# Kernel optimization log

Measured on AMD Instinct MI355X. Metric: run time of the kernel, lower is better.

Reference implementation:

```python
import jax, jax.numpy as jnp
import numpy as np

EPS = 1e-5

def gather_neighbour(pc, idx):
    # pc: [B,N,d], idx: [B,Q,k] -> [B,Q,k,d]
    return jax.vmap(lambda p, i: p[i])(pc, idx)

def rel_pos_encoding(q_xyz, src_xyz, idx):
    # q_xyz: [B,Q,3], src_xyz: [B,N,3], idx: [B,Q,k] -> [B,Q,k,10]
    nbr = gather_neighbour(src_xyz, idx)              # [B,Q,k,3]
    tile = q_xyz[:, :, None, :]                       # [B,Q,1,3]
    rel = tile - nbr                                  # [B,Q,k,3]
    dis = jnp.sqrt(jnp.sum(rel * rel, axis=-1, keepdims=True))
    tile_b = jnp.broadcast_to(tile, nbr.shape)
    return jnp.concatenate([dis, rel, tile_b, nbr], axis=-1)

def conv_bn_relu(x, W, g, b, m, v):
    # 1x1 conv (bias-free) + inference BatchNorm + ReLU; x: [B,Q,K,Cin], W: [Cout,Cin]
    y = jnp.einsum('bqkc,oc->bqko', x, W)
    y = (y - m) * (g * jax.lax.rsqrt(v + EPS)) + b
    return jax.nn.relu(y)

def att_pool(x, Wfc, Wm, g, b, m, v):
    # x: [B,Q,K,C] -> [B,Q,1,Cout]; softmax over neighbor axis K
    att = jnp.einsum('bqkc,oc->bqko', x, Wfc)
    att = jax.nn.softmax(att, axis=2)
    agg = jnp.sum(x * att, axis=2, keepdims=True)     # [B,Q,1,C]
    return conv_bn_relu(agg, Wm, g, b, m, v)

def setup_inputs() -> dict:
    key = jax.random.key(0)
    ks = jax.random.split(key, 40)
    B, Q, k, Nd, Ns = 2, 16384, 16, 4096, 16384
    dim_lb, dim_sc, dim_nl = 128, 64, 128
    d_mid = dim_lb + 10 - dim_sc   # 74
    d_att = dim_lb + 10            # 138
    f32 = jnp.float32
    inp = {}
    inp['features_lb'] = jax.random.normal(ks[0], (B, Q, k, dim_lb), f32)
    inp['features_sc'] = jax.random.normal(ks[1], (B, Q, k, dim_sc), f32)
    inp['NM_lb'] = jax.random.randint(ks[2], (B, Q, k), 0, Nd)
    inp['NM_sc'] = jax.random.randint(ks[3], (B, Q, k), 0, Ns)
    inp['coords_lb'] = jax.random.normal(ks[4], (B, Nd, 3), f32)
    inp['coords_sc'] = jax.random.normal(ks[5], (B, Ns, 3), f32)
    inp['coords_queries'] = jax.random.normal(ks[6], (B, Q, 3), f32)
    inp['NM_cl'] = jax.random.randint(ks[7], (B, Q, k), 0, Q)
    def bn(i, c):
        return (jax.random.uniform(ks[i], (c,), f32) + 0.5,
                jax.random.normal(ks[i + 1], (c,), f32) * 0.1,
                jax.random.normal(ks[i + 2], (c,), f32) * 0.1,
                jax.random.uniform(ks[i + 3], (c,), f32) + 0.5)
    inp['W_lb'] = jax.random.normal(ks[8], (10, 10), f32) * 0.3
    inp['g_lb'], inp['b_lb'], inp['m_lb'], inp['v_lb'] = bn(9, 10)
    inp['W_sc'] = jax.random.normal(ks[13], (d_mid, 10), f32) * 0.3
    inp['g_sc'], inp['b_sc'], inp['m_sc'], inp['v_sc'] = bn(14, d_mid)
    inp['W_fc1'] = jax.random.normal(ks[18], (d_att, d_att), f32) * 0.08
    inp['W_mlp1'] = jax.random.normal(ks[19], (dim_nl, d_att), f32) * 0.08
    inp['g1'], inp['b1'], inp['m1'], inp['v1'] = bn(20, dim_nl)
    inp['W_cl'] = jax.random.normal(ks[24], (10, 10), f32) * 0.3
    inp['g_cl'], inp['b_cl'], inp['m_cl'], inp['v_cl'] = bn(25, 10)
    inp['W_fc2'] = jax.random.normal(ks[29], (d_att, d_att), f32) * 0.08
    inp['W_mlp2'] = jax.random.normal(ks[30], (dim_nl, d_att), f32) * 0.08
    inp['g2'], inp['b2'], inp['m2'], inp['v2'] = bn(31, dim_nl)
    return inp

def reference(features_lb, features_sc, NM_lb, NM_sc, coords_lb, coords_sc,
              coords_queries, NM_cl,
              W_lb, g_lb, b_lb, m_lb, v_lb,
              W_sc, g_sc, b_sc, m_sc, v_sc,
              W_fc1, W_mlp1, g1, b1, m1, v1,
              W_cl, g_cl, b_cl, m_cl, v_cl,
              W_fc2, W_mlp2, g2, b2, m2, v2):
    # branch 1: layer-below
    rppe_lb = conv_bn_relu(rel_pos_encoding(coords_queries, coords_lb, NM_lb),
                           W_lb, g_lb, b_lb, m_lb, v_lb)          # [B,Q,k,10]
    # branch 2: skip connection
    rppe_sc = conv_bn_relu(rel_pos_encoding(coords_queries, coords_sc, NM_sc),
                           W_sc, g_sc, b_sc, m_sc, v_sc)          # [B,Q,k,74]
    locSE_lb = jnp.concatenate([rppe_lb, features_lb], axis=-1)   # [B,Q,k,138]
    locSE_sc = jnp.concatenate([rppe_sc, features_sc], axis=-1)   # [B,Q,k,138]
    f_hat = jnp.concatenate([locSE_lb, locSE_sc], axis=2)         # [B,Q,2k,138]
    f_tilde = att_pool(f_hat, W_fc1, W_mlp1, g1, b1, m1, v1)      # [B,Q,1,128]
    # second aggregation over current layer (num_agg > 1)
    rppe_cl = conv_bn_relu(rel_pos_encoding(coords_queries, coords_queries, NM_cl),
                           W_cl, g_cl, b_cl, m_cl, v_cl)          # [B,Q,k,10]
    f_cur = gather_neighbour(f_tilde[:, :, 0, :], NM_cl)          # [B,Q,k,128]
    locSE_cl = jnp.concatenate([rppe_cl, f_cur], axis=-1)         # [B,Q,k,138]
    f_tilde = att_pool(locSE_cl, W_fc2, W_mlp2, g2, b2, m2, v2)   # [B,Q,1,128]
    # match torch output layout [B, dim_nl, Q, 1]
    return jnp.transpose(f_tilde, (0, 3, 1, 2))
```

## Files before the change

### kernel.cpp

```cpp
#include <hip/hip_runtime.h>
#include <cmath>

#define EPSF 1e-5f
typedef unsigned int  uint32;
typedef unsigned short u16;
typedef __attribute__((ext_vector_type(8))) short bfrag;
typedef __attribute__((ext_vector_type(4))) float f32x4;

constexpr int Qn   = 16384;
constexpr int KS   = 168;
constexpr int PXS  = 42;
constexpr int AGS  = 168;
constexpr int Nd   = 4096;
constexpr float LOG2E = 1.4426950408889634f;

constexpr int OFF_W1  = 0;
constexpr int OFF_WM1 = 23040;
constexpr int OFF_W2  = 43520;
constexpr int OFF_WM2 = 66560;
constexpr int OFF_WLB = 87040;
constexpr int OFF_WSC = 87552;
constexpr int OFF_WCL = 90112;
constexpr int END_W   = 90624;
constexpr int BN_LB = 0;
constexpr int BN_SC = 20;
constexpr int BN_CL = 168;
constexpr int BN_M1 = 188;
constexpr int BN_M2 = 444;
constexpr int BN_TOT = 700;
constexpr int OFF_FT  = END_W + 2 * BN_TOT;
constexpr int PREP_N  = END_W + BN_TOT;

__device__ __forceinline__ u16 f2b(float f) {
    uint32 u = __float_as_uint(f);
    uint32 r = (u + 0x7fffu + ((u >> 16) & 1u)) >> 16;
    return (u16)r;
}
__device__ __forceinline__ float b2f(u16 h) {
    return __uint_as_float(((uint32)h) << 16);
}
__device__ __forceinline__ uint32 cvtpk(float a, float b) {
    uint32 r;
    asm("v_cvt_pk_bf16_f32 %0, %1, %2" : "=v"(r) : "v"(a), "v"(b));
    return r;
}
__device__ __forceinline__ u16 cvt1(float a) { return (u16)cvtpk(a, a); }
__device__ __forceinline__ float exp2_hw(float x) { return __builtin_amdgcn_exp2f(x); }

__global__ __launch_bounds__(256) void prep_weights(
    const float* __restrict__ Wfc1, const float* __restrict__ Wmlp1,
    const float* __restrict__ Wfc2, const float* __restrict__ Wmlp2,
    const float* __restrict__ Wlb,  const float* __restrict__ Wsc,
    const float* __restrict__ Wcl,
    const float* __restrict__ g_lb, const float* __restrict__ b_lb,
    const float* __restrict__ m_lb, const float* __restrict__ v_lb,
    const float* __restrict__ g_sc, const float* __restrict__ b_sc,
    const float* __restrict__ m_sc, const float* __restrict__ v_sc,
    const float* __restrict__ g_cl, const float* __restrict__ b_cl,
    const float* __restrict__ m_cl, const float* __restrict__ v_cl,
    const float* __restrict__ g1, const float* __restrict__ b1,
    const float* __restrict__ m1, const float* __restrict__ v1,
    const float* __restrict__ g2, const float* __restrict__ b2,
    const float* __restrict__ m2, const float* __restrict__ v2,
    u16* __restrict__ ws16)
{
    int i = blockIdx.x * 256 + threadIdx.x;
    if (i >= PREP_N) return;
    if (i >= END_W) {
        int j = i - END_W;
        const float *g, *bb, *m, *v; int o2;
        if (j < BN_SC)      { g = g_lb; bb = b_lb; m = m_lb; v = v_lb; o2 = j - BN_LB; }
        else if (j < BN_CL) { g = g_sc; bb = b_sc; m = m_sc; v = v_sc; o2 = j - BN_SC; }
        else if (j < BN_M1) { g = g_cl; bb = b_cl; m = m_cl; v = v_cl; o2 = j - BN_CL; }
        else if (j < BN_M2) { g = g1;   bb = b1;   m = m1;   v = v1;   o2 = j - BN_M1; }
        else                { g = g2;   bb = b2;   m = m2;   v = v2;   o2 = j - BN_M2; }
        int o = o2 >> 1;
        float sc_ = g[o] * rsqrtf(v[o] + EPSF);
        ((float*)(ws16 + END_W))[j] = (o2 & 1) ? (bb[o] - m[o] * sc_) : sc_;
        return;
    }
    int lane = (i >> 3) & 63, jj = i & 7;
    int row16 = lane & 15;
    int kf = ((lane >> 4) << 3) + jj;
    float v = 0.f;
    if (i < OFF_WLB) {
        const float* src; int nrows; int idx; bool fc = false;
        if (i < OFF_WM1)      { src = Wfc1;  nrows = 138; idx = i - OFF_W1;  fc = true; }
        else if (i < OFF_W2)  { src = Wmlp1; nrows = 128; idx = i - OFF_WM1; }
        else if (i < OFF_WM2) { src = Wfc2;  nrows = 138; idx = i - OFF_W2;  fc = true; }
        else                  { src = Wmlp2; nrows = 128; idx = i - OFF_WM2; }
        int t = idx >> 9, nt = t / 5, kt = t - nt * 5;
        int row = nt * 16 + row16;
        int kp  = kt * 32 + kf;
        int k   = (kp < 10) ? kp : kp - 2;
        if (row < nrows && kp < 140 && kp != 10 && kp != 11) {
            v = src[row * 138 + k];
            if (fc) v *= LOG2E;
        }
    } else {
        const float* src; int nrows; int idx;
        if (i < OFF_WSC)      { src = Wlb; nrows = 10; idx = i - OFF_WLB; }
        else if (i < OFF_WCL) { src = Wsc; nrows = 74; idx = i - OFF_WSC; }
        else                  { src = Wcl; nrows = 10; idx = i - OFF_WCL; }
        int t = idx >> 9;
        int row = t * 16 + row16;
        if (row < nrows && kf < 10) v = src[row * 10 + kf];
    }
    ws16[i] = f2b(v);
}

__device__ __forceinline__ void loadB(bfrag (&bf)[5], const u16* __restrict__ Wt,
                                      int nt, int lane) {
    #pragma unroll
    for (int kt = 0; kt < 5; ++kt)
        bf[kt] = *(const bfrag*)&Wt[((nt * 5 + kt) << 9) + (lane << 3)];
}
__device__ __forceinline__ void mfma32(const bfrag (&af)[2][5], const bfrag (&bf)[5],
                                       f32x4 &a0, f32x4 &a1) {
    const f32x4 zf = {0.f, 0.f, 0.f, 0.f};
    a0 = zf; a1 = zf;
    #pragma unroll
    for (int kt = 0; kt < 5; ++kt) {
        a0 = __builtin_amdgcn_mfma_f32_16x16x32_bf16(af[0][kt], bf[kt], a0, 0, 0, 0);
        a1 = __builtin_amdgcn_mfma_f32_16x16x32_bf16(af[1][kt], bf[kt], a1, 0, 0, 0);
    }
}
__device__ __forceinline__ void mfma16(const bfrag (&af)[5], const bfrag (&bf)[5],
                                       f32x4 &a0) {
    const f32x4 zf = {0.f, 0.f, 0.f, 0.f};
    a0 = zf;
    #pragma unroll
    for (int kt = 0; kt < 5; ++kt)
        a0 = __builtin_amdgcn_mfma_f32_16x16x32_bf16(af[kt], bf[kt], a0, 0, 0, 0);
}
__device__ __forceinline__ void soft32(
    const f32x4& a0, const f32x4& a1, int nt, int q,
    int lane, int lrow, int lgr, const u16* fh, u16* aggs)
{
    const int ch  = nt * 16 + lrow;
    const int chp = ch + (ch >= 10 ? 2 : 0);
    float s = 0.f, num = 0.f;
    #pragma unroll
    for (int r = 0; r < 4; ++r) {
        float e = exp2_hw(a0[r]);
        s += e;
        num += e * b2f(fh[(q * 32 + lgr * 4 + r) * KS + chp]);
    }
    #pragma unroll
    for (int r = 0; r < 4; ++r) {
        float e = exp2_hw(a1[r]);
        s += e;
        num += e * b2f(fh[(q * 32 + 16 + lgr * 4 + r) * KS + chp]);
    }
    s   += __shfl_xor(s, 16);   s   += __shfl_xor(s, 32);
    num += __shfl_xor(num, 16); num += __shfl_xor(num, 32);
    if (lane < 16)
        aggs[q * AGS + chp] = cvt1((ch < 138) ? num * __builtin_amdgcn_rcpf(s) : 0.f);
}
__device__ __forceinline__ void soft16(
    const f32x4& a0, int nt, int q,
    int lane, int lrow, int lgr, const u16* fh, u16* aggs)
{
    const int ch  = nt * 16 + lrow;
    const int chp = ch + (ch >= 10 ? 2 : 0);
    float s = 0.f, num = 0.f;
    #pragma unroll
    for (int r = 0; r < 4; ++r) {
        float e = exp2_hw(a0[r]);
        s += e;
        num += e * b2f(fh[(q * 16 + lgr * 4 + r) * KS + chp]);
    }
    s   += __shfl_xor(s, 16);   s   += __shfl_xor(s, 32);
    num += __shfl_xor(num, 16); num += __shfl_xor(num, 32);
    if (lane < 16)
        aggs[q * AGS + chp] = cvt1((ch < 138) ? num * __builtin_amdgcn_rcpf(s) : 0.f);
}
#define SB() __builtin_amdgcn_sched_barrier(0)

__global__ __launch_bounds__(256, 4) void stage1(
    const float* __restrict__ feat_lb, const float* __restrict__ feat_sc,
    const int* __restrict__ nm_lb, const int* __restrict__ nm_sc,
    const float* __restrict__ c_lb, const float* __restrict__ c_sc,
    const float* __restrict__ c_q,
    u16* __restrict__ ws16)
{
    __shared__ __align__(16) u16 fhat[64 * KS];
    __shared__ __align__(16) u16 pxs[64 * PXS];
    u16* aggs = pxs;

    const int tid  = threadIdx.x;
    const int bq0  = blockIdx.x * 2;
    const int b    = bq0 >> 14;
    const int lane = tid & 63;
    const int w    = tid >> 6;
    const int lrow = lane & 15;
    const int lgr  = lane >> 4;
    const int q    = w >> 1;
    const int h    = w & 1;

    const u16* W1t  = ws16 + OFF_W1;
    const u16* Wm1t = ws16 + OFF_WM1;
    const float* bn = (const float*)(ws16 + END_W);
    u16* ft = ws16 + OFF_FT;

    bfrag wcv[3];
    float2 bnv[3];
    if (h == 0) {
        wcv[0] = *(const bfrag*)&ws16[OFF_WLB + (lane << 3)];
        wcv[1] = *(const bfrag*)&ws16[OFF_WSC + (lane << 3)];
        wcv[2] = *(const bfrag*)&ws16[OFF_WSC + 512 + (lane << 3)];
        bnv[0] = (lrow < 10) ? *(const float2*)&bn[BN_LB + lrow * 2] : float2{0.f, 0.f};
        bnv[1] = *(const float2*)&bn[BN_SC + lrow * 2];
        bnv[2] = *(const float2*)&bn[BN_SC + (16 + lrow) * 2];
    } else {
        #pragma unroll
        for (int t = 0; t < 3; ++t) {
            wcv[t] = *(const bfrag*)&ws16[OFF_WSC + ((2 + t) << 9) + (lane << 3)];
            int o = (2 + t) * 16 + lrow;
            bnv[t] = (o < 74) ? *(const float2*)&bn[BN_SC + o * 2] : float2{0.f, 0.f};
        }
    }

    {
        const float4* flb = (const float4*)(feat_lb + (size_t)bq0 * 2048);
        float4 r0[4];
        #pragma unroll
        for (int it = 0; it < 4; ++it) r0[it] = flb[tid + it * 256];
        const float4* fsc = (const float4*)(feat_sc + (size_t)bq0 * 1024);
        float4 r1[2];
        #pragma unroll
        for (int it = 0; it < 2; ++it) r1[it] = fsc[tid + it * 256];
        #pragma unroll
        for (int it = 0; it < 4; ++it) {
            int u = tid + it * 256;
            int qq = u >> 9, rem = u & 511, r = rem >> 5, c4 = rem & 31;
            uint32* d = (uint32*)&fhat[(qq * 32 + r) * KS + 12 + c4 * 4];
            d[0] = cvtpk(r0[it].x, r0[it].y); d[1] = cvtpk(r0[it].z, r0[it].w);
        }
        #pragma unroll
        for (int it = 0; it < 2; ++it) {
            int u = tid + it * 256;
            int qq = u >> 8, rem = u & 255, r = rem >> 4, c4 = rem & 15;
            uint32* d = (uint32*)&fhat[(qq * 32 + 16 + r) * KS + 76 + c4 * 4];
            d[0] = cvtpk(r1[it].x, r1[it].y); d[1] = cvtpk(r1[it].z, r1[it].w);
        }
        for (int u = tid; u < 64 * 15; u += 256) {
            int row = u / 15, jj = u - row * 15;
            uint32* base = (uint32*)((char*)fhat + row * 336);
            if (jj == 0) base[5] = 0u; else base[69 + jj] = 0u;
        }
    }
    if (tid < 64) {
        const int qq = tid >> 5, r = tid & 31;
        const int bq = bq0 + qq;
        const bool lb = r < 16;
        const int idx = lb ? nm_lb[bq * 16 + r] : nm_sc[bq * 16 + (r - 16)];
        const float* nb = lb ? (c_lb + ((size_t)b * Nd + idx) * 3)
                             : (c_sc + ((size_t)b * Qn + idx) * 3);
        const float qx = c_q[bq * 3 + 0], qy = c_q[bq * 3 + 1], qz = c_q[bq * 3 + 2];
        const float nx = nb[0], ny = nb[1], nz = nb[2];
        const float rx = qx - nx, ry = qy - ny, rz = qz - nz;
        const float dd = sqrtf(rx * rx + ry * ry + rz * rz);
        uint32* pw = (uint32*)&pxs[tid * PXS];
        pw[0] = cvtpk(dd, rx); pw[1] = cvtpk(ry, rz); pw[2] = cvtpk(qx, qy);
        pw[3] = cvtpk(qz, nx); pw[4] = cvtpk(ny, nz);
        #pragma unroll
        for (int z = 5; z < 16; ++z) pw[z] = 0u;
    }
    __syncthreads();

    const f32x4 zf = {0.f, 0.f, 0.f, 0.f};

    {
        bfrag pa1 = *(const bfrag*)&pxs[(q * 32 + 16 + lrow) * PXS + lgr * 8];
        if (h == 0) {
            bfrag pa0 = *(const bfrag*)&pxs[(q * 32 + lrow) * PXS + lgr * 8];
            f32x4 c = __builtin_amdgcn_mfma_f32_16x16x32_bf16(pa0, wcv[0], zf, 0, 0, 0);
            if (lrow < 10) {
                #pragma unroll
                for (int r = 0; r < 4; ++r)
                    fhat[(q * 32 + lgr * 4 + r) * KS + lrow] =
                        cvt1(fmaxf(c[r] * bnv[0].x + bnv[0].y, 0.f));
            }
            #pragma unroll
            for (int t = 1; t < 3; ++t) {
                f32x4 c2 = __builtin_amdgcn_mfma_f32_16x16x32_bf16(pa1, wcv[t], zf, 0, 0, 0);
                const int o  = (t - 1) * 16 + lrow;
                const int cp = (o < 10) ? o : o + 2;
                #pragma unroll
                for (int r = 0; r < 4; ++r)
                    fhat[(q * 32 + 16 + lgr * 4 + r) * KS + cp] =
                        cvt1(fmaxf(c2[r] * bnv[t].x + bnv[t].y, 0.f));
            }
        } else {
            #pragma unroll
            for (int t = 0; t < 3; ++t) {
                f32x4 c2 = __builtin_amdgcn_mfma_f32_16x16x32_bf16(pa1, wcv[t], zf, 0, 0, 0);
                const int o = (2 + t) * 16 + lrow;
                if (o < 74) {
                    #pragma unroll
                    for (int r = 0; r < 4; ++r)
                        fhat[(q * 32 + 16 + lgr * 4 + r) * KS + o + 2] =
                            cvt1(fmaxf(c2[r] * bnv[t].x + bnv[t].y, 0.f));
                }
            }
        }
    }
    __syncthreads();

    bfrag af[2][5];
    #pragma unroll
    for (int mt = 0; mt < 2; ++mt)
        #pragma unroll
        for (int kt = 0; kt < 5; ++kt)
            af[mt][kt] = *(const bfrag*)&fhat[(q * 32 + mt * 16 + lrow) * KS + kt * 32 + lgr * 8];

    bfrag b0[5], b1[5];
    f32x4 a0, a1;
    if (h == 0) {
        loadB(b0, W1t, 0, lane);
        loadB(b1, W1t, 1, lane); mfma32(af, b0, a0, a1); SB(); soft32(a0, a1, 0, q, lane, lrow, lgr, fhat, aggs);
        loadB(b0, W1t, 2, lane); mfma32(af, b1, a0, a1); SB(); soft32(a0, a1, 1, q, lane, lrow, lgr, fhat, aggs);
        loadB(b1, W1t, 3, lane); mfma32(af, b0, a0, a1); SB(); soft32(a0, a1, 2, q, lane, lrow, lgr, fhat, aggs);
        loadB(b0, W1t, 4, lane); mfma32(af, b1, a0, a1); SB(); soft32(a0, a1, 3, q, lane, lrow, lgr, fhat, aggs);
        mfma32(af, b0, a0, a1); soft32(a0, a1, 4, q, lane, lrow, lgr, fhat, aggs);
        if (lane < 2)       aggs[q * AGS + 10 + lane] = 0;
        else if (lane < 16) aggs[q * AGS + 144 + lane] = 0;
    } else {
        loadB(b0, W1t, 5, lane);
        loadB(b1, W1t, 6, lane); mfma32(af, b0, a0, a1); SB(); soft32(a0, a1, 5, q, lane, lrow, lgr, fhat, aggs);
        loadB(b0, W1t, 7, lane); mfma32(af, b1, a0, a1); SB(); soft32(a0, a1, 6, q, lane, lrow, lgr, fhat, aggs);
        loadB(b1, W1t, 8, lane); mfma32(af, b0, a0, a1); SB(); soft32(a0, a1, 7, q, lane, lrow, lgr, fhat, aggs);
        mfma32(af, b1, a0, a1); soft32(a0, a1, 8, q, lane, lrow, lgr, fhat, aggs);
    }
    __syncthreads();

    bfrag am[5];
    #pragma unroll
    for (int kt = 0; kt < 5; ++kt)
        am[kt] = *(const bfrag*)&aggs[lrow * AGS + kt * 32 + lgr * 8];
    #pragma unroll
    for (int oi = 0; oi < 2; ++oi) {
        const int ot = w * 2 + oi;
        f32x4 c = zf;
        #pragma unroll
        for (int kt = 0; kt < 5; ++kt) {
            bfrag wm = *(const bfrag*)&Wm1t[(((ot * 5) + kt) << 9) + (lane << 3)];
            c = __builtin_amdgcn_mfma_f32_16x16x32_bf16(am[kt], wm, c, 0, 0, 0);
        }
        if (lgr == 0) {
            const int o = ot * 16 + lrow;
            float2 p = *(const float2*)&bn[BN_M1 + o * 2];
            #pragma unroll
            for (int r = 0; r < 2; ++r)
                ft[(size_t)(bq0 + r) * 128 + o] = cvt1(fmaxf(c[r] * p.x + p.y, 0.f));
        }
    }
}

__global__ __launch_bounds__(256, 4) void stage2(
    const int* __restrict__ nm_cl, const float* __restrict__ c_q,
    const u16* __restrict__ ws16, float* __restrict__ out)
{
    __shared__ __align__(16) u16 fhat[64 * KS];
    __shared__ __align__(16) u16 pxs[64 * PXS];
    u16* aggs = pxs;

    const int tid  = threadIdx.x;
    const int bq0  = blockIdx.x * 4;
    const int b    = bq0 >> 14;
    const int q0   = bq0 & (Qn - 1);
    const int lane = tid & 63;
    const int w    = tid >> 6;
    const int lrow = lane & 15;
    const int lgr  = lane >> 4;

    const u16* W2t  = ws16 + OFF_W2;
    const u16* Wm2t = ws16 + OFF_WM2;
    const float* bn = (const float*)(ws16 + END_W);
    const u16* ft   = ws16 + OFF_FT;

    bfrag wcl = *(const bfrag*)&ws16[OFF_WCL + (lane << 3)];
    float2 bncl = (lrow < 10) ? *(const float2*)&bn[BN_CL + lrow * 2] : float2{0.f, 0.f};

    for (int u = tid; u < 64 * 15; u += 256) {
        int row = u / 15, jj = u - row * 15;
        uint32* base = (uint32*)((char*)fhat + row * 336);
        if (jj == 0) base[5] = 0u; else base[69 + jj] = 0u;
    }
    if (tid < 64) {
        const int qq = tid >> 4, r = tid & 15;
        const int bq = bq0 + qq;
        const int idx = nm_cl[bq * 16 + r];
        const float* nb = c_q + ((size_t)(b << 14) + idx) * 3;
        const float qx = c_q[bq * 3 + 0], qy = c_q[bq * 3 + 1], qz = c_q[bq * 3 + 2];
        const float nx = nb[0], ny = nb[1], nz = nb[2];
        const float rx = qx - nx, ry = qy - ny, rz = qz - nz;
        const float dd = sqrtf(rx * rx + ry * ry + rz * rz);
        uint32* pw = (uint32*)&pxs[tid * PXS];
        pw[0] = cvtpk(dd, rx); pw[1] = cvtpk(ry, rz); pw[2] = cvtpk(qx, qy);
        pw[3] = cvtpk(qz, nx); pw[4] = cvtpk(ny, nz);
        #pragma unroll
        for (int z = 5; z < 16; ++z) pw[z] = 0u;
    }
    for (int u = tid; u < 4096; u += 256) {
        int row = u >> 6, c2 = u & 63;
        int qq = row >> 4;
        int idx = nm_cl[(bq0 + qq) * 16 + (row & 15)];
        const uint32* srow = (const uint32*)(ft + (size_t)((b << 14) + idx) * 128);
        *(uint32*)&fhat[row * KS + 12 + c2 * 2] = srow[c2];
    }
    __syncthreads();

    const f32x4 zf = {0.f, 0.f, 0.f, 0.f};

    {
        bfrag pa = *(const bfrag*)&pxs[(w * 16 + lrow) * PXS + lgr * 8];
        f32x4 c = __builtin_amdgcn_mfma_f32_16x16x32_bf16(pa, wcl, zf, 0, 0, 0);
        if (lrow < 10) {
            #pragma unroll
            for (int r = 0; r < 4; ++r)
                fhat[(w * 16 + lgr * 4 + r) * KS + lrow] =
                    cvt1(fmaxf(c[r] * bncl.x + bncl.y, 0.f));
        }
    }
    __syncthreads();

    bfrag af[5];
    #pragma unroll
    for (int kt = 0; kt < 5; ++kt)
        af[kt] = *(const bfrag*)&fhat[(w * 16 + lrow) * KS + kt * 32 + lgr * 8];

    bfrag b0[5], b1[5];
    f32x4 a0;
    loadB(b0, W2t, 0, lane);
    loadB(b1, W2t, 1, lane); mfma16(af, b0, a0); SB(); soft16(a0, 0, w, lane, lrow, lgr, fhat, aggs);
    loadB(b0, W2t, 2, lane); mfma16(af, b1, a0); SB(); soft16(a0, 1, w, lane, lrow, lgr, fhat, aggs);
    loadB(b1, W2t, 3, lane); mfma16(af, b0, a0); SB(); soft16(a0, 2, w, lane, lrow, lgr, fhat, aggs);
    loadB(b0, W2t, 4, lane); mfma16(af, b1, a0); SB(); soft16(a0, 3, w, lane, lrow, lgr, fhat, aggs);
    loadB(b1, W2t, 5, lane); mfma16(af, b0, a0); SB(); soft16(a0, 4, w, lane, lrow, lgr, fhat, aggs);
    loadB(b0, W2t, 6, lane); mfma16(af, b1, a0); SB(); soft16(a0, 5, w, lane, lrow, lgr, fhat, aggs);
    loadB(b1, W2t, 7, lane); mfma16(af, b0, a0); SB(); soft16(a0, 6, w, lane, lrow, lgr, fhat, aggs);
    loadB(b0, W2t, 8, lane); mfma16(af, b1, a0); SB(); soft16(a0, 7, w, lane, lrow, lgr, fhat, aggs);
    mfma16(af, b0, a0); soft16(a0, 8, w, lane, lrow, lgr, fhat, aggs);
    if (lane < 2)       aggs[w * AGS + 10 + lane] = 0;
    else if (lane < 16) aggs[w * AGS + 144 + lane] = 0;
    __syncthreads();

    bfrag am[5];
    #pragma unroll
    for (int kt = 0; kt < 5; ++kt)
        am[kt] = *(const bfrag*)&aggs[lrow * AGS + kt * 32 + lgr * 8];
    #pragma unroll
    for (int oi = 0; oi < 2; ++oi) {
        const int ot = w * 2 + oi;
        f32x4 c = zf;
        #pragma unroll
        for (int kt = 0; kt < 5; ++kt) {
            bfrag wm = *(const bfrag*)&Wm2t[(((ot * 5) + kt) << 9) + (lane << 3)];
            c = __builtin_amdgcn_mfma_f32_16x16x32_bf16(am[kt], wm, c, 0, 0, 0);
        }
        if (lgr == 0) {
            const int o = ot * 16 + lrow;
            float2 p = *(const float2*)&bn[BN_M2 + o * 2];
            #pragma unroll
            for (int r = 0; r < 4; ++r)
                out[((size_t)(b * 128 + o) << 14) + q0 + r] = fmaxf(c[r] * p.x + p.y, 0.f);
        }
    }
}

extern "C" void kernel_launch(void* const* d_in, const int* in_sizes, int n_in,
                              void* d_out, int out_size, void* d_ws, size_t ws_size,
                              hipStream_t stream)
{
    const float* feat_lb = (const float*)d_in[0];
    const float* feat_sc = (const float*)d_in[1];
    const int*   nm_lb   = (const int*)d_in[2];
    const int*   nm_sc   = (const int*)d_in[3];
    const float* c_lb    = (const float*)d_in[4];
    const float* c_sc    = (const float*)d_in[5];
    const float* c_q     = (const float*)d_in[6];
    const int*   nm_cl   = (const int*)d_in[7];
    const float* W_lb = (const float*)d_in[8];
    const float* g_lb = (const float*)d_in[9];
    const float* b_lb = (const float*)d_in[10];
    const float* m_lb = (const float*)d_in[11];
    const float* v_lb = (const float*)d_in[12];
    const float* W_sc = (const float*)d_in[13];
    const float* g_sc = (const float*)d_in[14];
    const float* b_sc = (const float*)d_in[15];
    const float* m_sc = (const float*)d_in[16];
    const float* v_sc = (const float*)d_in[17];
    const float* W_fc1  = (const float*)d_in[18];
    const float* W_mlp1 = (const float*)d_in[19];
    const float* g1 = (const float*)d_in[20];
    const float* b1 = (const float*)d_in[21];
    const float* m1 = (const float*)d_in[22];
    const float* v1 = (const float*)d_in[23];
    const float* W_cl = (const float*)d_in[24];
    const float* g_cl = (const float*)d_in[25];
    const float* b_cl = (const float*)d_in[26];
    const float* m_cl = (const float*)d_in[27];
    const float* v_cl = (const float*)d_in[28];
    const float* W_fc2  = (const float*)d_in[29];
    const float* W_mlp2 = (const float*)d_in[30];
    const float* g2 = (const float*)d_in[31];
    const float* b2 = (const float*)d_in[32];
    const float* m2 = (const float*)d_in[33];
    const float* v2 = (const float*)d_in[34];

    u16* ws16 = (u16*)d_ws;
    float* out = (float*)d_out;

    hipLaunchKernelGGL(prep_weights, dim3((PREP_N + 255) / 256), dim3(256), 0, stream,
        W_fc1, W_mlp1, W_fc2, W_mlp2, W_lb, W_sc, W_cl,
        g_lb, b_lb, m_lb, v_lb, g_sc, b_sc, m_sc, v_sc,
        g_cl, b_cl, m_cl, v_cl, g1, b1, m1, v1, g2, b2, m2, v2, ws16);

    hipLaunchKernelGGL(stage1, dim3(2 * Qn / 2), dim3(256), 0, stream,
        feat_lb, feat_sc, nm_lb, nm_sc, c_lb, c_sc, c_q, ws16);

    hipLaunchKernelGGL(stage2, dim3(2 * Qn / 4), dim3(256), 0, stream,
        nm_cl, c_q, ws16, out);
}
```

Measured before the change: 240.3 us.

## Double stage2 block to eight queries and hoist softmax row pointers

Stage2 now uses 512 threads and processes eight queries per block, doubling its shared-memory tiles. Each of the eight waves computes one 16-channel output tile of the final MLP over all eight queries, so the Wm2 weight loads are spread across more queries. The softmax helpers now take precomputed row pointers instead of recomputing indices from q and lgr. The larger block doubles LDS use per block and may lower occupancy or change how well work is balanced.

After: 225.3 us. 6.3% less time.

```diff
diff --git a/kernel.cpp b/kernel.cpp
--- a/kernel.cpp
+++ b/kernel.cpp
@@ -134,8 +134,9 @@
         a0 = __builtin_amdgcn_mfma_f32_16x16x32_bf16(af[kt], bf[kt], a0, 0, 0, 0);
 }
 __device__ __forceinline__ void soft32(
-    const f32x4& a0, const f32x4& a1, int nt, int q,
-    int lane, int lrow, int lgr, const u16* fh, u16* aggs)
+    const f32x4& a0, const f32x4& a1, int nt,
+    int lane, int lrow, const u16* __restrict__ fr0, const u16* __restrict__ fr1,
+    u16* __restrict__ ag)
 {
     const int ch  = nt * 16 + lrow;
     const int chp = ch + (ch >= 10 ? 2 : 0);
@@ -144,22 +145,22 @@
     for (int r = 0; r < 4; ++r) {
         float e = exp2_hw(a0[r]);
         s += e;
-        num += e * b2f(fh[(q * 32 + lgr * 4 + r) * KS + chp]);
+        num += e * b2f(fr0[r * KS + chp]);
     }
     #pragma unroll
     for (int r = 0; r < 4; ++r) {
         float e = exp2_hw(a1[r]);
         s += e;
-        num += e * b2f(fh[(q * 32 + 16 + lgr * 4 + r) * KS + chp]);
+        num += e * b2f(fr1[r * KS + chp]);
     }
     s   += __shfl_xor(s, 16);   s   += __shfl_xor(s, 32);
     num += __shfl_xor(num, 16); num += __shfl_xor(num, 32);
     if (lane < 16)
-        aggs[q * AGS + chp] = cvt1((ch < 138) ? num * __builtin_amdgcn_rcpf(s) : 0.f);
+        ag[chp] = cvt1((ch < 138) ? num * __builtin_amdgcn_rcpf(s) : 0.f);
 }
 __device__ __forceinline__ void soft16(
-    const f32x4& a0, int nt, int q,
-    int lane, int lrow, int lgr, const u16* fh, u16* aggs)
+    const f32x4& a0, int nt,
+    int lane, int lrow, const u16* __restrict__ fr0, u16* __restrict__ ag)
 {
     const int ch  = nt * 16 + lrow;
     const int chp = ch + (ch >= 10 ? 2 : 0);
@@ -168,12 +169,12 @@
     for (int r = 0; r < 4; ++r) {
         float e = exp2_hw(a0[r]);
         s += e;
-        num += e * b2f(fh[(q * 16 + lgr * 4 + r) * KS + chp]);
+        num += e * b2f(fr0[r * KS + chp]);
     }
     s   += __shfl_xor(s, 16);   s   += __shfl_xor(s, 32);
     num += __shfl_xor(num, 16); num += __shfl_xor(num, 32);
     if (lane < 16)
-        aggs[q * AGS + chp] = cvt1((ch < 138) ? num * __builtin_amdgcn_rcpf(s) : 0.f);
+        ag[chp] = cvt1((ch < 138) ? num * __builtin_amdgcn_rcpf(s) : 0.f);
 }
 #define SB() __builtin_amdgcn_sched_barrier(0)
 
@@ -315,23 +316,27 @@
         for (int kt = 0; kt < 5; ++kt)
             af[mt][kt] = *(const bfrag*)&fhat[(q * 32 + mt * 16 + lrow) * KS + kt * 32 + lgr * 8];
 
+    const u16* fr0 = fhat + (q * 32 + lgr * 4) * KS;
+    const u16* fr1 = fr0 + 16 * KS;
+    u16* ag = aggs + q * AGS;
+
     bfrag b0[5], b1[5];
     f32x4 a0, a1;
     if (h == 0) {
         loadB(b0, W1t, 0, lane);
-        loadB(b1, W1t, 1, lane); mfma32(af, b0, a0, a1); SB(); soft32(a0, a1, 0, q, lane, lrow, lgr, fhat, aggs);
-        loadB(b0, W1t, 2, lane); mfma32(af, b1, a0, a1); SB(); soft32(a0, a1, 1, q, lane, lrow, lgr, fhat, aggs);
-        loadB(b1, W1t, 3, lane); mfma32(af, b0, a0, a1); SB(); soft32(a0, a1, 2, q, lane, lrow, lgr, fhat, aggs);
-        loadB(b0, W1t, 4, lane); mfma32(af, b1, a0, a1); SB(); soft32(a0, a1, 3, q, lane, lrow, lgr, fhat, aggs);
-        mfma32(af, b0, a0, a1); soft32(a0, a1, 4, q, lane, lrow, lgr, fhat, aggs);
-        if (lane < 2)       aggs[q * AGS + 10 + lane] = 0;
-        else if (lane < 16) aggs[q * AGS + 144 + lane] = 0;
+        loadB(b1, W1t, 1, lane); mfma32(af, b0, a0, a1); SB(); soft32(a0, a1, 0, lane, lrow, fr0, fr1, ag);
+        loadB(b0, W1t, 2, lane); mfma32(af, b1, a0, a1); SB(); soft32(a0, a1, 1, lane, lrow, fr0, fr1, ag);
+        loadB(b1, W1t, 3, lane); mfma32(af, b0, a0, a1); SB(); soft32(a0, a1, 2, lane, lrow, fr0, fr1, ag);
+        loadB(b0, W1t, 4, lane); mfma32(af, b1, a0, a1); SB(); soft32(a0, a1, 3, lane, lrow, fr0, fr1, ag);
+        mfma32(af, b0, a0, a1); soft32(a0, a1, 4, lane, lrow, fr0, fr1, ag);
+        if (lane < 2)       ag[10 + lane] = 0;
+        else if (lane < 16) ag[144 + lane] = 0;
     } else {
         loadB(b0, W1t, 5, lane);
-        loadB(b1, W1t, 6, lane); mfma32(af, b0, a0, a1); SB(); soft32(a0, a1, 5, q, lane, lrow, lgr, fhat, aggs);
-        loadB(b0, W1t, 7, lane); mfma32(af, b1, a0, a1); SB(); soft32(a0, a1, 6, q, lane, lrow, lgr, fhat, aggs);
-        loadB(b1, W1t, 8, lane); mfma32(af, b0, a0, a1); SB(); soft32(a0, a1, 7, q, lane, lrow, lgr, fhat, aggs);
-        mfma32(af, b1, a0, a1); soft32(a0, a1, 8, q, lane, lrow, lgr, fhat, aggs);
+        loadB(b1, W1t, 6, lane); mfma32(af, b0, a0, a1); SB(); soft32(a0, a1, 5, lane, lrow, fr0, fr1, ag);
+        loadB(b0, W1t, 7, lane); mfma32(af, b1, a0, a1); SB(); soft32(a0, a1, 6, lane, lrow, fr0, fr1, ag);
+        loadB(b1, W1t, 8, lane); mfma32(af, b0, a0, a1); SB(); soft32(a0, a1, 7, lane, lrow, fr0, fr1, ag);
+        mfma32(af, b1, a0, a1); soft32(a0, a1, 8, lane, lrow, fr0, fr1, ag);
     }
     __syncthreads();
 
@@ -358,16 +363,16 @@
     }
 }
 
-__global__ __launch_bounds__(256, 4) void stage2(
+__global__ __launch_bounds__(512, 4) void stage2(
     const int* __restrict__ nm_cl, const float* __restrict__ c_q,
     const u16* __restrict__ ws16, float* __restrict__ out)
 {
-    __shared__ __align__(16) u16 fhat[64 * KS];
-    __shared__ __align__(16) u16 pxs[64 * PXS];
+    __shared__ __align__(16) u16 fhat[128 * KS];
+    __shared__ __align__(16) u16 pxs[128 * PXS];
     u16* aggs = pxs;
 
     const int tid  = threadIdx.x;
-    const int bq0  = blockIdx.x * 4;
+    const int bq0  = blockIdx.x * 8;
     const int b    = bq0 >> 14;
     const int q0   = bq0 & (Qn - 1);
     const int lane = tid & 63;
@@ -383,12 +388,12 @@
     bfrag wcl = *(const bfrag*)&ws16[OFF_WCL + (lane << 3)];
     float2 bncl = (lrow < 10) ? *(const float2*)&bn[BN_CL + lrow * 2] : float2{0.f, 0.f};
 
-    for (int u = tid; u < 64 * 15; u += 256) {
+    for (int u = tid; u < 128 * 15; u += 512) {
         int row = u / 15, jj = u - row * 15;
         uint32* base = (uint32*)((char*)fhat + row * 336);
         if (jj == 0) base[5] = 0u; else base[69 + jj] = 0u;
     }
-    if (tid < 64) {
+    if (tid < 128) {
         const int qq = tid >> 4, r = tid & 15;
         const int bq = bq0 + qq;
         const int idx = nm_cl[bq * 16 + r];
@@ -403,7 +408,9 @@
         #pragma unroll
         for (int z = 5; z < 16; ++z) pw[z] = 0u;
     }
-    for (int u = tid; u < 4096; u += 256) {
+    #pragma unroll
+    for (int i = 0; i < 16; ++i) {
+        int u = tid + i * 512;
         int row = u >> 6, c2 = u & 63;
         int qq = row >> 4;
         int idx = nm_cl[(bq0 + qq) * 16 + (row & 15)];
@@ -431,41 +438,44 @@
     for (int kt = 0; kt < 5; ++kt)
         af[kt] = *(const bfrag*)&fhat[(w * 16 + lrow) * KS + kt * 32 + lgr * 8];
 
+    const u16* fr0 = fhat + (w * 16 + lgr * 4) * KS;
+    u16* ag = aggs + w * AGS;
+
     bfrag b0[5], b1[5];
     f32x4 a0;
     loadB(b0, W2t, 0, lane);
-    loadB(b1, W2t, 1, lane); mfma16(af, b0, a0); SB(); soft16(a0, 0, w, lane, lrow, lgr, fhat, aggs);
-    loadB(b0, W2t, 2, lane); mfma16(af, b1, a0); SB(); soft16(a0, 1, w, lane, lrow, lgr, fhat, aggs);
-    loadB(b1, W2t, 3, lane); mfma16(af, b0, a0); SB(); soft16(a0, 2, w, lane, lrow, lgr, fhat, aggs);
-    loadB(b0, W2t, 4, lane); mfma16(af, b1, a0); SB(); soft16(a0, 3, w, lane, lrow, lgr, fhat, aggs);
-    loadB(b1, W2t, 5, lane); mfma16(af, b0, a0); SB(); soft16(a0, 4, w, lane, lrow, lgr, fhat, aggs);
-    loadB(b0, W2t, 6, lane); mfma16(af, b1, a0); SB(); soft16(a0, 5, w, lane, lrow, lgr, fhat, aggs);
-    loadB(b1, W2t, 7, lane); mfma16(af, b0, a0); SB(); soft16(a0, 6, w, lane, lrow, lgr, fhat, aggs);
-    loadB(b0, W2t, 8, lane); mfma16(af, b1, a0); SB(); soft16(a0, 7, w, lane, lrow, lgr, fhat, aggs);
-    mfma16(af, b0, a0); soft16(a0, 8, w, lane, lrow, lgr, fhat, aggs);
-    if (lane < 2)       aggs[w * AGS + 10 + lane] = 0;
-    else if (lane < 16) aggs[w * AGS + 144 + lane] = 0;
+    loadB(b1, W2t, 1, lane); mfma16(af, b0, a0); SB(); soft16(a0, 0, lane, lrow, fr0, ag);
+    loadB(b0, W2t, 2, lane); mfma16(af, b1, a0); SB(); soft16(a0, 1, lane, lrow, fr0, ag);
+    loadB(b1, W2t, 3, lane); mfma16(af, b0, a0); SB(); soft16(a0, 2, lane, lrow, fr0, ag);
+    loadB(b0, W2t, 4, lane); mfma16(af, b1, a0); SB(); soft16(a0, 3, lane, lrow, fr0, ag);
+    loadB(b1, W2t, 5, lane); mfma16(af, b0, a0); SB(); soft16(a0, 4, lane, lrow, fr0, ag);
+    loadB(b0, W2t, 6, lane); mfma16(af, b1, a0); SB(); soft16(a0, 5, lane, lrow, fr0, ag);
+    loadB(b1, W2t, 7, lane); mfma16(af, b0, a0); SB(); soft16(a0, 6, lane, lrow, fr0, ag);
+    loadB(b0, W2t, 8, lane); mfma16(af, b1, a0); SB(); soft16(a0, 7, lane, lrow, fr0, ag);
+    mfma16(af, b0, a0); soft16(a0, 8, lane, lrow, fr0, ag);
+    if (lane < 2)       ag[10 + lane] = 0;
+    else if (lane < 16) ag[144 + lane] = 0;
     __syncthreads();
 
     bfrag am[5];
     #pragma unroll
     for (int kt = 0; kt < 5; ++kt)
         am[kt] = *(const bfrag*)&aggs[lrow * AGS + kt * 32 + lgr * 8];
-    #pragma unroll
-    for (int oi = 0; oi < 2; ++oi) {
-        const int ot = w * 2 + oi;
+    {
         f32x4 c = zf;
         #pragma unroll
         for (int kt = 0; kt < 5; ++kt) {
-            bfrag wm = *(const bfrag*)&Wm2t[(((ot * 5) + kt) << 9) + (lane << 3)];
+            bfrag wm = *(const bfrag*)&Wm2t[(((w * 5) + kt) << 9) + (lane << 3)];
             c = __builtin_amdgcn_mfma_f32_16x16x32_bf16(am[kt], wm, c, 0, 0, 0);
         }
-        if (lgr == 0) {
-            const int o = ot * 16 + lrow;
+        if (lgr < 2) {
+            const int o = w * 16 + lrow;
             float2 p = *(const float2*)&bn[BN_M2 + o * 2];
             #pragma unroll
-            for (int r = 0; r < 4; ++r)
-                out[((size_t)(b * 128 + o) << 14) + q0 + r] = fmaxf(c[r] * p.x + p.y, 0.f);
+            for (int r = 0; r < 4; ++r) {
+                const int qloc = lgr * 4 + r;
+                out[((size_t)(b * 128 + o) << 14) + q0 + qloc] = fmaxf(c[r] * p.x + p.y, 0.f);
+            }
         }
     }
 }
@@ -521,6 +531,6 @@
     hipLaunchKernelGGL(stage1, dim3(2 * Qn / 2), dim3(256), 0, stream,
         feat_lb, feat_sc, nm_lb, nm_sc, c_lb, c_sc, c_q, ws16);
 
-    hipLaunchKernelGGL(stage2, dim3(2 * Qn / 4), dim3(256), 0, stream,
+    hipLaunchKernelGGL(stage2, dim3(2 * Qn / 8), dim3(512), 0, stream,
         nm_cl, c_q, ws16, out);
 }
```
